# Kernel tuning notes

Measured on AMD Instinct MI355X. Metric: run time of the kernel, lower is better.

## Reference

```python
import jax, jax.numpy as jnp
import numpy as np

BEAM = 64
RANK = 32
VOCAB = 21128


def setup_inputs() -> dict:
    key = jax.random.key(0)
    k1, k2, k3, k4 = jax.random.split(key, 4)
    B, S, V = 16, 256, VOCAB
    emissions = jax.random.normal(k1, (B, S, V), jnp.float32)
    targets = jax.random.randint(k2, (B, S), 0, V)
    mask = jnp.ones((B, S), dtype=bool)
    E1 = jax.random.normal(k3, (V, RANK), jnp.float32) * 0.02
    E2 = jax.random.normal(k4, (V, RANK), jnp.float32) * 0.02
    return {"emissions": emissions, "targets": targets, "mask": mask, "E1": E1, "E2": E2}


def _crf_llh(emissions, targets, mask, E1, E2, beam=BEAM):
    B, S, V = emissions.shape
    maskf = mask.astype(emissions.dtype)

    # ---- numerator: score of the target path ----
    em = jnp.take_along_axis(emissions, targets[:, :, None], axis=2)[:, :, 0]  # [B,S]
    trans = jnp.sum(E1[targets[:, :-1]] * E2[targets[:, 1:]], axis=2)          # [B,S-1]
    scores = em.at[:, 1:].add(trans)
    numerator = jnp.sum(scores * maskf, axis=1)                                # [B]

    # ---- denominator: beam-approximated normalizer ----
    # force target token into the beam (scatter +inf, then topk indices)
    b_idx = jnp.arange(B)[:, None]
    s_idx = jnp.arange(S)[None, :]
    _em = emissions.at[b_idx, s_idx, targets].set(jnp.inf)
    _, beam_targets = jax.lax.top_k(_em, beam)                                 # [B,S,beam]
    beam_em = jnp.take_along_axis(emissions, beam_targets, axis=2)             # [B,S,beam]

    t1 = E1[beam_targets[:, :-1]]                                              # [B,S-1,beam,rank]
    t2 = E2[beam_targets[:, 1:]]                                               # [B,S-1,beam,rank]
    beam_trans = jnp.einsum('bsir,bsjr->bsij', t1, t2)                         # [B,S-1,beam,beam]

    score0 = beam_em[:, 0]                                                     # [B,beam]

    def step(score, x):
        trans_i, emit_i, m_i = x
        nxt = jax.scipy.special.logsumexp(score[:, :, None] + trans_i, axis=1) + emit_i
        score = jnp.where(m_i[:, None], nxt, score)
        return score, None

    xs = (jnp.swapaxes(beam_trans, 0, 1),          # [S-1,B,beam,beam]
          jnp.swapaxes(beam_em[:, 1:], 0, 1),      # [S-1,B,beam]
          jnp.swapaxes(mask[:, 1:], 0, 1))         # [S-1,B]
    score, _ = jax.lax.scan(step, score0, xs)
    denominator = jax.scipy.special.logsumexp(score, axis=1)                   # [B]

    llh = numerator - denominator
    return jnp.sum(llh)  # reduction='sum'


def reference(emissions, targets, mask, E1, E2):
    return _crf_llh(emissions, targets, mask, E1, E2)
```

## Files before the change

kernel.cpp:

```cpp
#include <hip/hip_runtime.h>
#include <stdint.h>

#define Bn 16
#define Sn 256
#define Vn 21128
#define NV4 5282
#define RANKn 32
#define BEAMn 64
#define HBINS 4096
#define CAPn 512
#define NSEG 16
#define LOG2E 1.44269504088896340736f
#define LN2   0.69314718055994530942f

#define EXP2F(x) __builtin_amdgcn_exp2f(x)
#define LOG2F(x) __builtin_amdgcn_logf(x)

__device__ __forceinline__ unsigned f2o(unsigned b) {
    return (b & 0x80000000u) ? ~b : (b | 0x80000000u);
}
__device__ __forceinline__ float o2f(unsigned u) {
    unsigned b = (u & 0x80000000u) ? (u ^ 0x80000000u) : ~u;
    return __uint_as_float(b);
}
__device__ __forceinline__ float dot4(float4 a, float4 b) {
    return a.x * b.x + a.y * b.y + a.z * b.z + a.w * b.w;
}

__global__ __launch_bounds__(256) void topk_kernel(const float* __restrict__ emis,
                                                   const int* __restrict__ targets,
                                                   int* __restrict__ beam_idx,
                                                   float* __restrict__ beam_val) {
    const int row = blockIdx.x;
    const float* __restrict__ rowp = emis + (size_t)row * Vn;
    const int tgt = targets[row];
    __shared__ unsigned hist[HBINS];
    __shared__ unsigned csum[256];
    __shared__ unsigned cu[CAPn];
    __shared__ int      cix[CAPn];
    __shared__ int      selidx[BEAMn];
    __shared__ float    selval[BEAMn];
    __shared__ unsigned ccount;
    __shared__ int      binstar;
    __shared__ int      chunkc;
    __shared__ int      hastgt;
    __shared__ unsigned wcnt[4];
    const int t = threadIdx.x;
    if (t == 0) { ccount = 0; hastgt = 0; }

    const unsigned THRU = f2o(__float_as_uint(2.5f));
    uint4 vals[21];
    unsigned cntl = 0;
    #pragma unroll
    for (int it = 0; it < 21; ++it) {
        int v4 = t + it * 256;
        if (v4 < NV4) {
            const uint4 raw = ((const uint4*)rowp)[v4];
            uint4 u;
            u.x = f2o(raw.x); u.y = f2o(raw.y); u.z = f2o(raw.z); u.w = f2o(raw.w);
            vals[it] = u;
            cntl += (u.x > THRU) + (u.y > THRU) + (u.z > THRU) + (u.w > THRU);
        }
    }
    for (int off = 32; off; off >>= 1) cntl += __shfl_xor(cntl, off, 64);
    if ((t & 63) == 0) wcnt[t >> 6] = cntl;
    __syncthreads();
    const unsigned C0 = wcnt[0] + wcnt[1] + wcnt[2] + wcnt[3];

    if (C0 >= BEAMn && C0 <= CAPn) {
        #pragma unroll
        for (int it = 0; it < 21; ++it) {
            int v4 = t + it * 256;
            if (v4 < NV4) {
                uint4 u = vals[it];
                int bi = v4 * 4;
                if (u.x > THRU) { unsigned p = atomicAdd(&ccount, 1u); cu[p] = u.x; cix[p] = bi;     }
                if (u.y > THRU) { unsigned p = atomicAdd(&ccount, 1u); cu[p] = u.y; cix[p] = bi + 1; }
                if (u.z > THRU) { unsigned p = atomicAdd(&ccount, 1u); cu[p] = u.z; cix[p] = bi + 2; }
                if (u.w > THRU) { unsigned p = atomicAdd(&ccount, 1u); cu[p] = u.w; cix[p] = bi + 3; }
            }
        }
    } else {
        for (int i = t; i < HBINS; i += 256) hist[i] = 0;
        __syncthreads();
        #pragma unroll
        for (int it = 0; it < 21; ++it) {
            int v4 = t + it * 256;
            if (v4 < NV4) {
                uint4 u = vals[it];
                atomicAdd(&hist[u.x >> 20], 1u);
                atomicAdd(&hist[u.y >> 20], 1u);
                atomicAdd(&hist[u.z >> 20], 1u);
                atomicAdd(&hist[u.w >> 20], 1u);
            }
        }
        __syncthreads();
        unsigned cs = 0;
        #pragma unroll
        for (int i = 0; i < 16; ++i) cs += hist[t * 16 + i];
        csum[t] = cs;
        __syncthreads();
        for (int off = 1; off < 256; off <<= 1) {
            unsigned v = csum[t] + ((t + off < 256) ? csum[t + off] : 0u);
            __syncthreads();
            csum[t] = v;
            __syncthreads();
        }
        if (csum[t] >= BEAMn && (t == 255 || csum[t + 1] < BEAMn)) chunkc = t;
        __syncthreads();
        if (t == 0) {
            int tc = chunkc;
            unsigned acc = (tc == 255) ? 0u : csum[tc + 1];
            int bs = tc * 16;
            for (int b2 = tc * 16 + 15; b2 >= tc * 16; --b2) {
                acc += hist[b2];
                if (acc >= BEAMn) { bs = b2; break; }
            }
            binstar = bs;
        }
        __syncthreads();
        const unsigned bstar = (unsigned)binstar;
        #pragma unroll
        for (int it = 0; it < 21; ++it) {
            int v4 = t + it * 256;
            if (v4 < NV4) {
                uint4 u = vals[it];
                int bi = v4 * 4;
                if ((u.x >> 20) >= bstar) { unsigned p = atomicAdd(&ccount, 1u); if (p < CAPn) { cu[p] = u.x; cix[p] = bi;     } }
                if ((u.y >> 20) >= bstar) { unsigned p = atomicAdd(&ccount, 1u); if (p < CAPn) { cu[p] = u.y; cix[p] = bi + 1; } }
                if ((u.z >> 20) >= bstar) { unsigned p = atomicAdd(&ccount, 1u); if (p < CAPn) { cu[p] = u.z; cix[p] = bi + 2; } }
                if ((u.w >> 20) >= bstar) { unsigned p = atomicAdd(&ccount, 1u); if (p < CAPn) { cu[p] = u.w; cix[p] = bi + 3; } }
            }
        }
    }
    __syncthreads();
    const int C = (int)min(ccount, (unsigned)CAPn);
    for (int p = t; p < C; p += 256) {
        unsigned up = cu[p]; int ip = cix[p];
        int rank = 0;
        for (int q = 0; q < C; ++q) {
            unsigned uq = cu[q];
            rank += (uq > up) || (uq == up && cix[q] < ip);
        }
        if (rank < BEAMn) { selidx[rank] = ip; selval[rank] = o2f(up); }
    }
    __syncthreads();
    if (t < BEAMn && selidx[t] == tgt) hastgt = 1;
    __syncthreads();
    if (t == 0 && !hastgt) { selidx[BEAMn - 1] = tgt; selval[BEAMn - 1] = rowp[tgt]; }
    __syncthreads();
    if (t < BEAMn) {
        beam_idx[(size_t)row * BEAMn + t] = selidx[t];
        beam_val[(size_t)row * BEAMn + t] = selval[t];
    }
}

#define TPAD 68
__global__ __launch_bounds__(256) void trans_kernel(const float* __restrict__ E1,
                                                    const float* __restrict__ E2,
                                                    const int* __restrict__ beam_idx,
                                                    float* __restrict__ trans) {
    const int blk = blockIdx.x;
    const int b = blk / (Sn - 1);
    const int k = blk - b * (Sn - 1);
    const int* bi = beam_idx + ((size_t)(b * Sn + k)) * BEAMn;
    const int* bj = beam_idx + ((size_t)(b * Sn + k + 1)) * BEAMn;
    __shared__ float e1t[RANKn][TPAD];
    __shared__ float e2t[RANKn][TPAD];
    const int t = threadIdx.x;
    {
        const int row = t >> 2, q = t & 3;
        const int rb = q * 8;
        int i1 = bi[row];
        const float4* s1 = (const float4*)(E1 + (size_t)i1 * RANKn) + q * 2;
        float4 a0 = s1[0], a1 = s1[1];
        e1t[rb + 0][row] = a0.x; e1t[rb + 1][row] = a0.y; e1t[rb + 2][row] = a0.z; e1t[rb + 3][row] = a0.w;
        e1t[rb + 4][row] = a1.x; e1t[rb + 5][row] = a1.y; e1t[rb + 6][row] = a1.z; e1t[rb + 7][row] = a1.w;
        int i2 = bj[row];
        const float4* s2 = (const float4*)(E2 + (size_t)i2 * RANKn) + q * 2;
        float4 b0 = s2[0], b1 = s2[1];
        e2t[rb + 0][row] = b0.x; e2t[rb + 1][row] = b0.y; e2t[rb + 2][row] = b0.z; e2t[rb + 3][row] = b0.w;
        e2t[rb + 4][row] = b1.x; e2t[rb + 5][row] = b1.y; e2t[rb + 6][row] = b1.z; e2t[rb + 7][row] = b1.w;
    }
    __syncthreads();
    const int ti = t & 15, tj = t >> 4;
    const int i0 = ti * 4, j0 = tj * 4;
    float acc[4][4] = {};
    #pragma unroll
    for (int r = 0; r < RANKn; ++r) {
        float4 a = *(const float4*)&e1t[r][i0];
        float4 bb = *(const float4*)&e2t[r][j0];
        acc[0][0] += a.x * bb.x; acc[0][1] += a.x * bb.y; acc[0][2] += a.x * bb.z; acc[0][3] += a.x * bb.w;
        acc[1][0] += a.y * bb.x; acc[1][1] += a.y * bb.y; acc[1][2] += a.y * bb.z; acc[1][3] += a.y * bb.w;
        acc[2][0] += a.z * bb.x; acc[2][1] += a.z * bb.y; acc[2][2] += a.z * bb.z; acc[2][3] += a.z * bb.w;
        acc[3][0] += a.w * bb.x; acc[3][1] += a.w * bb.y; acc[3][2] += a.w * bb.z; acc[3][3] += a.w * bb.w;
    }
    float* outp = trans + (size_t)blk * (BEAMn * BEAMn);
    #pragma unroll
    for (int ii = 0; ii < 4; ++ii) {
        float4 o = { EXP2F(acc[ii][0] * LOG2E), EXP2F(acc[ii][1] * LOG2E),
                     EXP2F(acc[ii][2] * LOG2E), EXP2F(acc[ii][3] * LOG2E) };
        *(float4*)&outp[(i0 + ii) * BEAMn + j0] = o;
    }
}

__global__ __launch_bounds__(256) void segprod_kernel(const float* __restrict__ trans,
                                                      const float* __restrict__ beam_val,
                                                      const int* __restrict__ mask,
                                                      float* __restrict__ segP,
                                                      float* __restrict__ segL) {
    const int blk = blockIdx.x;
    const int b = blk >> 4, s = blk & 15;
    const int k0 = s * 16;
    const int nk = min(16, (Sn - 1) - k0);
    const float* __restrict__ trb = trans + ((size_t)b * (Sn - 1) + k0) * (BEAMn * BEAMn);
    const float* __restrict__ bv  = beam_val + (size_t)b * Sn * BEAMn;
    const int* __restrict__ mk = mask + (size_t)b * Sn;
    __shared__ float Qa[64][64], Qb[64][64], Mld[64][64];
    __shared__ float ev[16][64];
    __shared__ int   mvec[16];
    __shared__ float wmax[4];
    const int t = threadIdx.x;
    const int ti = t & 15, tj = t >> 4;
    const int i0 = ti * 4, j0 = tj * 4;

    for (int x = t; x < 4096; x += 256)
        (&Qa[0][0])[x] = ((x >> 6) == (x & 63)) ? 1.f : 0.f;
    for (int x = t; x < nk * 64; x += 256)
        ev[x >> 6][x & 63] = EXP2F(bv[(size_t)(k0 + (x >> 6) + 1) * BEAMn + (x & 63)] * LOG2E);
    if (t < nk) mvec[t] = mk[k0 + t + 1];
    __syncthreads();

    float (*Qc)[64] = Qa, (*Qn)[64] = Qb;
    float L = 0.f;
    for (int kk = 0; kk < nk; ++kk) {
        const float4* Ms = (const float4*)(trb + (size_t)kk * (BEAMn * BEAMn));
        #pragma unroll
        for (int q = 0; q < 4; ++q) {
            int p = t + q * 256;
            int r = p >> 4, cc = (p & 15) * 4;
            float4 v = Ms[p];
            float4 e = *(const float4*)&ev[kk][cc];
            v.x *= e.x; v.y *= e.y; v.z *= e.z; v.w *= e.w;
            *(float4*)&Mld[r][cc] = v;
        }
        __syncthreads();
        const int live = mvec[kk];
        float acc[4][4];
        if (live) {
            #pragma unroll
            for (int ii = 0; ii < 4; ++ii)
                #pragma unroll
                for (int jj = 0; jj < 4; ++jj) acc[ii][jj] = 0.f;
            for (int r = 0; r < 64; ++r) {
                float4 a  = *(const float4*)&Qc[r][i0];
                float4 bb = *(const float4*)&Mld[r][j0];
                acc[0][0] += a.x * bb.x; acc[0][1] += a.x * bb.y; acc[0][2] += a.x * bb.z; acc[0][3] += a.x * bb.w;
                acc[1][0] += a.y * bb.x; acc[1][1] += a.y * bb.y; acc[1][2] += a.y * bb.z; acc[1][3] += a.y * bb.w;
                acc[2][0] += a.z * bb.x; acc[2][1] += a.z * bb.y; acc[2][2] += a.z * bb.z; acc[2][3] += a.z * bb.w;
                acc[3][0] += a.w * bb.x; acc[3][1] += a.w * bb.y; acc[3][2] += a.w * bb.z; acc[3][3] += a.w * bb.w;
            }
            float lm = acc[0][0];
            #pragma unroll
            for (int ii = 0; ii < 4; ++ii)
                #pragma unroll
                for (int jj = 0; jj < 4; ++jj) lm = fmaxf(lm, acc[ii][jj]);
            for (int off = 32; off; off >>= 1) lm = fmaxf(lm, __shfl_xor(lm, off, 64));
            if ((t & 63) == 0) wmax[t >> 6] = lm;
        }
        __syncthreads();
        if (live) {
            const float m = fmaxf(fmaxf(wmax[0], wmax[1]), fmaxf(wmax[2], wmax[3]));
            const float inv = 1.f / m;
            #pragma unroll
            for (int jj = 0; jj < 4; ++jj) {
                float4 w = { acc[0][jj] * inv, acc[1][jj] * inv, acc[2][jj] * inv, acc[3][jj] * inv };
                *(float4*)&Qn[j0 + jj][i0] = w;
            }
            L += LOG2F(m);
            float (*tmp)[64] = Qc; Qc = Qn; Qn = tmp;
        }
        __syncthreads();
    }
    float* op = segP + (size_t)blk * 4096;
    for (int x = t; x < 4096; x += 256) op[x] = (&Qc[0][0])[x];
    if (t == 0) segL[blk] = L;
}

__global__ __launch_bounds__(256) void finale_kernel(const float* __restrict__ segP,
                                                     const float* __restrict__ segL,
                                                     const float* __restrict__ beam_val,
                                                     float* __restrict__ out) {
    const int b = blockIdx.x;
    const int t = threadIdx.x;
    const int w = t >> 6, j = t & 63;
    const float* __restrict__ bv = beam_val + (size_t)b * Sn * BEAMn;
    __shared__ float us[BEAMn];
    __shared__ float part[4][BEAMn + 1];
    float sc = bv[j] * LOG2E;
    float mx = sc;
    for (int off = 32; off; off >>= 1) mx = fmaxf(mx, __shfl_xor(mx, off, 64));
    float u = EXP2F(sc - mx);
    float Ltot = mx;
    const float* p0 = segP + ((size_t)b * NSEG) * 4096 + (size_t)j * 64 + w * 16;
    float4 ra0 = ((const float4*)p0)[0], ra1 = ((const float4*)p0)[1],
           ra2 = ((const float4*)p0)[2], ra3 = ((const float4*)p0)[3];
    for (int s2 = 0; s2 < NSEG; ++s2) {
        float4 rb0, rb1, rb2, rb3;
        if (s2 + 1 < NSEG) {
            const float* pn = segP + ((size_t)b * NSEG + s2 + 1) * 4096 + (size_t)j * 64 + w * 16;
            rb0 = ((const float4*)pn)[0]; rb1 = ((const float4*)pn)[1];
            rb2 = ((const float4*)pn)[2]; rb3 = ((const float4*)pn)[3];
        }
        if (w == 0) us[j] = u;
        __syncthreads();
        const float4* uu = (const float4*)&us[w * 16];
        float a2 = dot4(ra0, uu[0]) + dot4(ra1, uu[1]) + dot4(ra2, uu[2]) + dot4(ra3, uu[3]);
        part[w][j] = a2;
        __syncthreads();
        float tot = part[0][j] + part[1][j] + part[2][j] + part[3][j];
        float m = tot;
        for (int off = 32; off; off >>= 1) m = fmaxf(m, __shfl_xor(m, off, 64));
        u = tot / m;
        Ltot += LOG2F(m) + segL[b * NSEG + s2];
        ra0 = rb0; ra1 = rb1; ra2 = rb2; ra3 = rb3;
    }
    if (t < BEAMn) {
        float e = u;
        for (int off = 32; off; off >>= 1) e += __shfl_xor(e, off, 64);
        if (t == 0) atomicAdd(out, -LN2 * (Ltot + LOG2F(e)));
    }
}

__global__ __launch_bounds__(256) void num_kernel(const float* __restrict__ emis,
                                                  const int* __restrict__ targets,
                                                  const int* __restrict__ mask,
                                                  const float* __restrict__ E1,
                                                  const float* __restrict__ E2,
                                                  float* __restrict__ out) {
    const int gid = blockIdx.x * 256 + threadIdx.x;
    float val = 0.f;
    if (gid < Bn * Sn) {
        int s = gid & (Sn - 1);
        int tg = targets[gid];
        float em = emis[(size_t)gid * Vn + tg];
        float tr = 0.f;
        if (s > 0) {
            int pv = targets[gid - 1];
            const float4* p1 = (const float4*)(E1 + (size_t)pv * RANKn);
            const float4* p2 = (const float4*)(E2 + (size_t)tg * RANKn);
            #pragma unroll
            for (int r = 0; r < 8; ++r) {
                float4 a = p1[r], bb = p2[r];
                tr += a.x * bb.x + a.y * bb.y + a.z * bb.z + a.w * bb.w;
            }
        }
        if (mask[gid]) val = em + tr;
    }
    for (int off = 32; off; off >>= 1) val += __shfl_xor(val, off, 64);
    __shared__ float wsum[4];
    if ((threadIdx.x & 63) == 0) wsum[threadIdx.x >> 6] = val;
    __syncthreads();
    if (threadIdx.x == 0) atomicAdd(out, wsum[0] + wsum[1] + wsum[2] + wsum[3]);
}

extern "C" void kernel_launch(void* const* d_in, const int* in_sizes, int n_in,
                              void* d_out, int out_size, void* d_ws, size_t ws_size,
                              hipStream_t stream) {
    const float* emis    = (const float*)d_in[0];
    const int*   targets = (const int*)d_in[1];
    const int*   mask    = (const int*)d_in[2];
    const float* E1      = (const float*)d_in[3];
    const float* E2      = (const float*)d_in[4];
    float* out = (float*)d_out;
    char* ws = (char*)d_ws;
    int*   beam_idx = (int*)ws;
    float* beam_val = (float*)(ws + (1 << 20));
    float* trans    = (float*)(ws + (2 << 20));
    float* segP     = (float*)(ws + ((size_t)69 << 20));
    float* segL     = (float*)(ws + ((size_t)74 << 20));

    (void)hipMemsetAsync(out, 0, sizeof(float), stream);
    hipLaunchKernelGGL(topk_kernel, dim3(Bn * Sn), dim3(256), 0, stream,
                       emis, targets, beam_idx, beam_val);
    hipLaunchKernelGGL(trans_kernel, dim3(Bn * (Sn - 1)), dim3(256), 0, stream,
                       E1, E2, beam_idx, trans);
    hipLaunchKernelGGL(num_kernel, dim3((Bn * Sn + 255) / 256), dim3(256), 0, stream,
                       emis, targets, mask, E1, E2, out);
    hipLaunchKernelGGL(segprod_kernel, dim3(Bn * NSEG), dim3(256), 0, stream,
                       trans, beam_val, mask, segP, segL);
    hipLaunchKernelGGL(finale_kernel, dim3(Bn), dim3(256), 0, stream,
                       segP, segL, beam_val, out);
}
```

Measured before the change: 573.5 us.

## Fuse transition computation into segment product kernel and numerator into topk

Stops materializing the exponentiated beam transition matrices in global memory. Each segment-product block now gathers the E1/E2 beam rows, computes the 64x64 rank-32 product, and folds in the emission exponent directly in shared memory. The numerator computation moves into the topk kernel's thread 0, which removes two kernel launches and the large trans round trip through HBM. In exchange the transition GEMM now runs inside the serial per-segment loop with an extra barrier per step, and the segment kernel launches only 256 blocks.

```diff
diff --git a/kernel.cpp b/kernel.cpp
--- a/kernel.cpp
+++ b/kernel.cpp
@@ -29,8 +29,12 @@
 
 __global__ __launch_bounds__(256) void topk_kernel(const float* __restrict__ emis,
                                                    const int* __restrict__ targets,
+                                                   const int* __restrict__ mask,
+                                                   const float* __restrict__ E1,
+                                                   const float* __restrict__ E2,
                                                    int* __restrict__ beam_idx,
-                                                   float* __restrict__ beam_val) {
+                                                   float* __restrict__ beam_val,
+                                                   float* __restrict__ out) {
     const int row = blockIdx.x;
     const float* __restrict__ rowp = emis + (size_t)row * Vn;
     const int tgt = targets[row];
@@ -153,58 +157,29 @@
         beam_idx[(size_t)row * BEAMn + t] = selidx[t];
         beam_val[(size_t)row * BEAMn + t] = selval[t];
     }
+    if (t == 0) {
+        const int s = row & (Sn - 1);
+        float val = 0.f;
+        if (mask[row]) {
+            float em = rowp[tgt];
+            float tr = 0.f;
+            if (s > 0) {
+                int pv = targets[row - 1];
+                const float4* p1 = (const float4*)(E1 + (size_t)pv * RANKn);
+                const float4* p2 = (const float4*)(E2 + (size_t)tgt * RANKn);
+                #pragma unroll
+                for (int r = 0; r < 8; ++r) tr += dot4(p1[r], p2[r]);
+            }
+            val = em + tr;
+        }
+        atomicAdd(out, val);
+    }
 }
 
 #define TPAD 68
-__global__ __launch_bounds__(256) void trans_kernel(const float* __restrict__ E1,
-                                                    const float* __restrict__ E2,
-                                                    const int* __restrict__ beam_idx,
-                                                    float* __restrict__ trans) {
-    const int blk = blockIdx.x;
-    const int b = blk / (Sn - 1);
-    const int k = blk - b * (Sn - 1);
-    const int* bi = beam_idx + ((size_t)(b * Sn + k)) * BEAMn;
-    const int* bj = beam_idx + ((size_t)(b * Sn + k + 1)) * BEAMn;
-    __shared__ float e1t[RANKn][TPAD];
-    __shared__ float e2t[RANKn][TPAD];
-    const int t = threadIdx.x;
-    {
-        const int row = t >> 2, q = t & 3;
-        const int rb = q * 8;
-        int i1 = bi[row];
-        const float4* s1 = (const float4*)(E1 + (size_t)i1 * RANKn) + q * 2;
-        float4 a0 = s1[0], a1 = s1[1];
-        e1t[rb + 0][row] = a0.x; e1t[rb + 1][row] = a0.y; e1t[rb + 2][row] = a0.z; e1t[rb + 3][row] = a0.w;
-        e1t[rb + 4][row] = a1.x; e1t[rb + 5][row] = a1.y; e1t[rb + 6][row] = a1.z; e1t[rb + 7][row] = a1.w;
-        int i2 = bj[row];
-        const float4* s2 = (const float4*)(E2 + (size_t)i2 * RANKn) + q * 2;
-        float4 b0 = s2[0], b1 = s2[1];
-        e2t[rb + 0][row] = b0.x; e2t[rb + 1][row] = b0.y; e2t[rb + 2][row] = b0.z; e2t[rb + 3][row] = b0.w;
-        e2t[rb + 4][row] = b1.x; e2t[rb + 5][row] = b1.y; e2t[rb + 6][row] = b1.z; e2t[rb + 7][row] = b1.w;
-    }
-    __syncthreads();
-    const int ti = t & 15, tj = t >> 4;
-    const int i0 = ti * 4, j0 = tj * 4;
-    float acc[4][4] = {};
-    #pragma unroll
-    for (int r = 0; r < RANKn; ++r) {
-        float4 a = *(const float4*)&e1t[r][i0];
-        float4 bb = *(const float4*)&e2t[r][j0];
-        acc[0][0] += a.x * bb.x; acc[0][1] += a.x * bb.y; acc[0][2] += a.x * bb.z; acc[0][3] += a.x * bb.w;
-        acc[1][0] += a.y * bb.x; acc[1][1] += a.y * bb.y; acc[1][2] += a.y * bb.z; acc[1][3] += a.y * bb.w;
-        acc[2][0] += a.z * bb.x; acc[2][1] += a.z * bb.y; acc[2][2] += a.z * bb.z; acc[2][3] += a.z * bb.w;
-        acc[3][0] += a.w * bb.x; acc[3][1] += a.w * bb.y; acc[3][2] += a.w * bb.z; acc[3][3] += a.w * bb.w;
-    }
-    float* outp = trans + (size_t)blk * (BEAMn * BEAMn);
-    #pragma unroll
-    for (int ii = 0; ii < 4; ++ii) {
-        float4 o = { EXP2F(acc[ii][0] * LOG2E), EXP2F(acc[ii][1] * LOG2E),
-                     EXP2F(acc[ii][2] * LOG2E), EXP2F(acc[ii][3] * LOG2E) };
-        *(float4*)&outp[(i0 + ii) * BEAMn + j0] = o;
-    }
-}
-
-__global__ __launch_bounds__(256) void segprod_kernel(const float* __restrict__ trans,
+__global__ __launch_bounds__(256) void segprod_kernel(const float* __restrict__ E1,
+                                                      const float* __restrict__ E2,
+                                                      const int* __restrict__ beam_idx,
                                                       const float* __restrict__ beam_val,
                                                       const int* __restrict__ mask,
                                                       float* __restrict__ segP,
@@ -213,11 +188,14 @@
     const int b = blk >> 4, s = blk & 15;
     const int k0 = s * 16;
     const int nk = min(16, (Sn - 1) - k0);
-    const float* __restrict__ trb = trans + ((size_t)b * (Sn - 1) + k0) * (BEAMn * BEAMn);
     const float* __restrict__ bv  = beam_val + (size_t)b * Sn * BEAMn;
-    const int* __restrict__ mk = mask + (size_t)b * Sn;
-    __shared__ float Qa[64][64], Qb[64][64], Mld[64][64];
-    __shared__ float ev[16][64];
+    const int* __restrict__ mk   = mask + (size_t)b * Sn;
+    const int* __restrict__ bidx = beam_idx + (size_t)b * Sn * BEAMn;
+    __shared__ float Qa[64][64], Qb[64][64];
+    __shared__ float Mld[64][68];
+    __shared__ float e1t[RANKn][TPAD];
+    __shared__ float e2t[RANKn][TPAD];
+    __shared__ float elog[16][64];
     __shared__ int   mvec[16];
     __shared__ float wmax[4];
     const int t = threadIdx.x;
@@ -227,25 +205,49 @@
     for (int x = t; x < 4096; x += 256)
         (&Qa[0][0])[x] = ((x >> 6) == (x & 63)) ? 1.f : 0.f;
     for (int x = t; x < nk * 64; x += 256)
-        ev[x >> 6][x & 63] = EXP2F(bv[(size_t)(k0 + (x >> 6) + 1) * BEAMn + (x & 63)] * LOG2E);
+        elog[x >> 6][x & 63] = bv[(size_t)(k0 + (x >> 6) + 1) * BEAMn + (x & 63)] * LOG2E;
     if (t < nk) mvec[t] = mk[k0 + t + 1];
     __syncthreads();
 
     float (*Qc)[64] = Qa, (*Qn)[64] = Qb;
     float L = 0.f;
+    const int srow = t >> 2, sq = t & 3;
     for (int kk = 0; kk < nk; ++kk) {
-        const float4* Ms = (const float4*)(trb + (size_t)kk * (BEAMn * BEAMn));
-        #pragma unroll
-        for (int q = 0; q < 4; ++q) {
-            int p = t + q * 256;
-            int r = p >> 4, cc = (p & 15) * 4;
-            float4 v = Ms[p];
-            float4 e = *(const float4*)&ev[kk][cc];
-            v.x *= e.x; v.y *= e.y; v.z *= e.z; v.w *= e.w;
-            *(float4*)&Mld[r][cc] = v;
-        }
-        __syncthreads();
         const int live = mvec[kk];
+        if (live) {
+            const int rb = sq * 8;
+            int i1 = bidx[(size_t)(k0 + kk) * BEAMn + srow];
+            const float4* s1 = (const float4*)(E1 + (size_t)i1 * RANKn) + sq * 2;
+            float4 a0 = s1[0], a1 = s1[1];
+            int i2 = bidx[(size_t)(k0 + kk + 1) * BEAMn + srow];
+            const float4* s2 = (const float4*)(E2 + (size_t)i2 * RANKn) + sq * 2;
+            float4 b0 = s2[0], b1 = s2[1];
+            e1t[rb + 0][srow] = a0.x; e1t[rb + 1][srow] = a0.y; e1t[rb + 2][srow] = a0.z; e1t[rb + 3][srow] = a0.w;
+            e1t[rb + 4][srow] = a1.x; e1t[rb + 5][srow] = a1.y; e1t[rb + 6][srow] = a1.z; e1t[rb + 7][srow] = a1.w;
+            e2t[rb + 0][srow] = b0.x; e2t[rb + 1][srow] = b0.y; e2t[rb + 2][srow] = b0.z; e2t[rb + 3][srow] = b0.w;
+            e2t[rb + 4][srow] = b1.x; e2t[rb + 5][srow] = b1.y; e2t[rb + 6][srow] = b1.z; e2t[rb + 7][srow] = b1.w;
+        }
+        __syncthreads();
+        if (live) {
+            float macc[4][4] = {};
+            #pragma unroll
+            for (int r = 0; r < RANKn; ++r) {
+                float4 a  = *(const float4*)&e1t[r][i0];
+                float4 bb = *(const float4*)&e2t[r][j0];
+                macc[0][0] += a.x * bb.x; macc[0][1] += a.x * bb.y; macc[0][2] += a.x * bb.z; macc[0][3] += a.x * bb.w;
+                macc[1][0] += a.y * bb.x; macc[1][1] += a.y * bb.y; macc[1][2] += a.y * bb.z; macc[1][3] += a.y * bb.w;
+                macc[2][0] += a.z * bb.x; macc[2][1] += a.z * bb.y; macc[2][2] += a.z * bb.z; macc[2][3] += a.z * bb.w;
+                macc[3][0] += a.w * bb.x; macc[3][1] += a.w * bb.y; macc[3][2] += a.w * bb.z; macc[3][3] += a.w * bb.w;
+            }
+            const float4 el = *(const float4*)&elog[kk][j0];
+            #pragma unroll
+            for (int ii = 0; ii < 4; ++ii) {
+                float4 o = { EXP2F(macc[ii][0] * LOG2E + el.x), EXP2F(macc[ii][1] * LOG2E + el.y),
+                             EXP2F(macc[ii][2] * LOG2E + el.z), EXP2F(macc[ii][3] * LOG2E + el.w) };
+                *(float4*)&Mld[i0 + ii][j0] = o;
+            }
+        }
+        __syncthreads();
         float acc[4][4];
         if (live) {
             #pragma unroll
@@ -332,38 +334,6 @@
     }
 }
 
-__global__ __launch_bounds__(256) void num_kernel(const float* __restrict__ emis,
-                                                  const int* __restrict__ targets,
-                                                  const int* __restrict__ mask,
-                                                  const float* __restrict__ E1,
-                                                  const float* __restrict__ E2,
-                                                  float* __restrict__ out) {
-    const int gid = blockIdx.x * 256 + threadIdx.x;
-    float val = 0.f;
-    if (gid < Bn * Sn) {
-        int s = gid & (Sn - 1);
-        int tg = targets[gid];
-        float em = emis[(size_t)gid * Vn + tg];
-        float tr = 0.f;
-        if (s > 0) {
-            int pv = targets[gid - 1];
-            const float4* p1 = (const float4*)(E1 + (size_t)pv * RANKn);
-            const float4* p2 = (const float4*)(E2 + (size_t)tg * RANKn);
-            #pragma unroll
-            for (int r = 0; r < 8; ++r) {
-                float4 a = p1[r], bb = p2[r];
-                tr += a.x * bb.x + a.y * bb.y + a.z * bb.z + a.w * bb.w;
-            }
-        }
-        if (mask[gid]) val = em + tr;
-    }
-    for (int off = 32; off; off >>= 1) val += __shfl_xor(val, off, 64);
-    __shared__ float wsum[4];
-    if ((threadIdx.x & 63) == 0) wsum[threadIdx.x >> 6] = val;
-    __syncthreads();
-    if (threadIdx.x == 0) atomicAdd(out, wsum[0] + wsum[1] + wsum[2] + wsum[3]);
-}
-
 extern "C" void kernel_launch(void* const* d_in, const int* in_sizes, int n_in,
                               void* d_out, int out_size, void* d_ws, size_t ws_size,
                               hipStream_t stream) {
@@ -376,19 +346,14 @@
     char* ws = (char*)d_ws;
     int*   beam_idx = (int*)ws;
     float* beam_val = (float*)(ws + (1 << 20));
-    float* trans    = (float*)(ws + (2 << 20));
-    float* segP     = (float*)(ws + ((size_t)69 << 20));
-    float* segL     = (float*)(ws + ((size_t)74 << 20));
+    float* segP     = (float*)(ws + (2 << 20));
+    float* segL     = (float*)(ws + (7 << 20));
 
     (void)hipMemsetAsync(out, 0, sizeof(float), stream);
     hipLaunchKernelGGL(topk_kernel, dim3(Bn * Sn), dim3(256), 0, stream,
-                       emis, targets, beam_idx, beam_val);
-    hipLaunchKernelGGL(trans_kernel, dim3(Bn * (Sn - 1)), dim3(256), 0, stream,
-                       E1, E2, beam_idx, trans);
-    hipLaunchKernelGGL(num_kernel, dim3((Bn * Sn + 255) / 256), dim3(256), 0, stream,
-                       emis, targets, mask, E1, E2, out);
+                       emis, targets, mask, E1, E2, beam_idx, beam_val, out);
     hipLaunchKernelGGL(segprod_kernel, dim3(Bn * NSEG), dim3(256), 0, stream,
-                       trans, beam_val, mask, segP, segL);
+                       E1, E2, beam_idx, beam_val, mask, segP, segL);
     hipLaunchKernelGGL(finale_kernel, dim3(Bn), dim3(256), 0, stream,
                        segP, segL, beam_val, out);
 }
```

After: 583.0 us. About the same (+1.7%).
